# Kernel tuning notes

Measured on AMD Instinct MI355X. Metric: run time of the kernel, lower is better.

## Reference

```python
import jax, jax.numpy as jnp
import numpy as np

T = 10
NUM_HEADS = 12

def _rel_pos_index(t):
    coords = jnp.arange(t)
    return coords[:, None] - coords[None, :] + (t - 1)  # [T, T] in [0, 2T-2]

def setup_inputs() -> dict:
    key = jax.random.key(0)
    ks = jax.random.split(key, 6)
    dim, attn_dim = 384, 384
    B_ = 16384
    return {
        "x": jax.random.normal(ks[0], (B_, T, dim), dtype=jnp.float32),
        "qkv_w": jax.random.normal(ks[1], (3 * attn_dim, dim), dtype=jnp.float32) * 0.02,
        "qkv_b": jax.random.normal(ks[2], (3 * attn_dim,), dtype=jnp.float32) * 0.02,
        "proj_w": jax.random.normal(ks[3], (dim, attn_dim), dtype=jnp.float32) * 0.02,
        "proj_b": jax.random.normal(ks[4], (dim,), dtype=jnp.float32) * 0.02,
        "bias_table": jax.random.normal(ks[5], (2 * T - 1, NUM_HEADS), dtype=jnp.float32) * 0.02,
    }

def reference(x, qkv_w, qkv_b, proj_w, proj_b, bias_table):
    B_, N, C = x.shape
    H = NUM_HEADS
    Dh = qkv_w.shape[0] // (3 * H)
    scale = Dh ** -0.5
    qkv = x @ qkv_w.T + qkv_b                       # [B_, N, 3*H*Dh]
    qkv = qkv.reshape(B_, N, 3, H, Dh).transpose(2, 0, 3, 1, 4)
    q, k, v = qkv[0], qkv[1], qkv[2]                # each [B_, H, N, Dh]
    idx = _rel_pos_index(N)                         # [N, N]
    bias = bias_table[idx].transpose(2, 0, 1)       # [H, N, N]
    attn = jnp.einsum('bhnd,bhmd->bhnm', q * scale, k) + bias[None]
    attn = jax.nn.softmax(attn, axis=-1)
    out = jnp.einsum('bhnm,bhmd->bhnd', attn, v)    # [B_, H, N, Dh]
    out = out.transpose(0, 2, 1, 3).reshape(B_, N, H * Dh)
    return out @ proj_w.T + proj_b
```

## Files before the change

kernel.cpp:

```cpp
#include <hip/hip_runtime.h>
#include <cstdint>
#include <cstddef>

#define T_TOK 10
#define NH 12
#define DH 32
#define DIM 384
#define QKVDIM 1152
#define NB 4
#define MROWS 40
#define XS_LD 392
#define QKV_LD 1160
#define SCALE 0.17677669529663689f

#define LDS_BYTES 131344

typedef short bf16x8 __attribute__((ext_vector_type(8)));
typedef float f32x4  __attribute__((ext_vector_type(4)));

__device__ __forceinline__ unsigned short f2b(float f) {
    unsigned u = __float_as_uint(f);
    u = (u + 0x7FFFu + ((u >> 16) & 1u)) >> 16;
    return (unsigned short)u;
}
__device__ __forceinline__ float b2f(unsigned short h) {
    return __uint_as_float(((unsigned)h) << 16);
}
__device__ __forceinline__ unsigned pack2(float a, float b) {
    return (unsigned)f2b(a) | ((unsigned)f2b(b) << 16);
}

__global__ void convert_weights(const float* __restrict__ qkv_w,
                                const float* __restrict__ proj_w,
                                unsigned short* __restrict__ wq,
                                unsigned short* __restrict__ wp) {
    int i = blockIdx.x * blockDim.x + threadIdx.x;
    const int N1 = QKVDIM * DIM / 4;
    const int N2 = DIM * DIM / 4;
    if (i < N1) {
        float4 v = ((const float4*)qkv_w)[i];
        uint2 o; o.x = pack2(v.x, v.y); o.y = pack2(v.z, v.w);
        ((uint2*)wq)[i] = o;
    } else if (i < N1 + N2) {
        int j = i - N1;
        float4 v = ((const float4*)proj_w)[j];
        uint2 o; o.x = pack2(v.x, v.y); o.y = pack2(v.z, v.w);
        ((uint2*)wp)[j] = o;
    }
}

extern __shared__ char smem[];

__global__ __launch_bounds__(256, 1) void fused_attn(
    const float* __restrict__ x,
    const float* __restrict__ qkv_b,
    const float* __restrict__ proj_b,
    const float* __restrict__ bias_table,
    const unsigned short* __restrict__ wq,
    const unsigned short* __restrict__ wp,
    float* __restrict__ out)
{
    const int t    = threadIdx.x;
    const int wg   = blockIdx.x;
    const int wave = t >> 6;
    const int lane = t & 63;
    const int quad = lane >> 4;
    const int l16  = lane & 15;

    unsigned short* xs       = (unsigned short*)smem;
    unsigned short* qkvs     = (unsigned short*)(smem + 37632);
    float*          outstage = (float*)(smem + 37632);
    float*          bias_lds = (float*)(smem + 130432);

    {
        const float4* x4 = (const float4*)(x + (size_t)wg * MROWS * DIM);
        #pragma unroll
        for (int i = 0; i < 15; ++i) {
            int idx = i * 256 + t;
            int row = idx / 96, c4 = idx % 96;
            float4 v = x4[idx];
            uint2 o; o.x = pack2(v.x, v.y); o.y = pack2(v.z, v.w);
            *(uint2*)(xs + row * XS_LD + c4 * 4) = o;
        }
        for (int idx = t; idx < 8 * 98; idx += 256) {
            int row = MROWS + idx / 98, c4 = idx % 98;
            *(uint2*)(xs + row * XS_LD + c4 * 4) = make_uint2(0u, 0u);
        }
        if (t < (2 * T_TOK - 1) * NH) bias_lds[t] = bias_table[t];
    }
    __syncthreads();

    {
        #pragma unroll 1
        for (int g = 0; g < 6; ++g) {
            f32x4 acc[3][3] = {};
            #pragma unroll
            for (int kc = 0; kc < 12; ++kc) {
                int koff = kc * 32 + quad * 8;
                bf16x8 a0 = *(const bf16x8*)(xs + ( 0 + l16) * XS_LD + koff);
                bf16x8 a1 = *(const bf16x8*)(xs + (16 + l16) * XS_LD + koff);
                bf16x8 a2 = *(const bf16x8*)(xs + (32 + l16) * XS_LD + koff);
                bf16x8 b0 = *(const bf16x8*)(wq + (size_t)((wave + 4*(3*g+0))*16 + l16) * DIM + koff);
                bf16x8 b1 = *(const bf16x8*)(wq + (size_t)((wave + 4*(3*g+1))*16 + l16) * DIM + koff);
                bf16x8 b2 = *(const bf16x8*)(wq + (size_t)((wave + 4*(3*g+2))*16 + l16) * DIM + koff);
                acc[0][0] = __builtin_amdgcn_mfma_f32_16x16x32_bf16(a0, b0, acc[0][0], 0, 0, 0);
                acc[0][1] = __builtin_amdgcn_mfma_f32_16x16x32_bf16(a0, b1, acc[0][1], 0, 0, 0);
                acc[0][2] = __builtin_amdgcn_mfma_f32_16x16x32_bf16(a0, b2, acc[0][2], 0, 0, 0);
                acc[1][0] = __builtin_amdgcn_mfma_f32_16x16x32_bf16(a1, b0, acc[1][0], 0, 0, 0);
                acc[1][1] = __builtin_amdgcn_mfma_f32_16x16x32_bf16(a1, b1, acc[1][1], 0, 0, 0);
                acc[1][2] = __builtin_amdgcn_mfma_f32_16x16x32_bf16(a1, b2, acc[1][2], 0, 0, 0);
                acc[2][0] = __builtin_amdgcn_mfma_f32_16x16x32_bf16(a2, b0, acc[2][0], 0, 0, 0);
                acc[2][1] = __builtin_amdgcn_mfma_f32_16x16x32_bf16(a2, b1, acc[2][1], 0, 0, 0);
                acc[2][2] = __builtin_amdgcn_mfma_f32_16x16x32_bf16(a2, b2, acc[2][2], 0, 0, 0);
            }
            #pragma unroll
            for (int j = 0; j < 3; ++j) {
                int n = (wave + 4*(3*g+j)) * 16 + l16;
                float qb = qkv_b[n];
                float sc = (n < DIM) ? SCALE : 1.0f;
                #pragma unroll
                for (int mt = 0; mt < 3; ++mt) {
                    #pragma unroll
                    for (int r = 0; r < 4; ++r) {
                        int m = mt * 16 + quad * 4 + r;
                        if (m < MROWS)
                            qkvs[m * QKV_LD + n] = f2b((acc[mt][j][r] + qb) * sc);
                    }
                }
            }
        }
    }
    __syncthreads();

    if (t < 240) {
        int pr = t / 5, rp = t % 5;
        int bl = pr / NH, h = pr % NH;
        int m0 = bl * T_TOK + rp * 2;
        int ti0 = rp * 2, ti1 = rp * 2 + 1;

        float q0[DH], q1[DH];
        const unsigned* qp0 = (const unsigned*)(qkvs + m0 * QKV_LD + h * DH);
        const unsigned* qp1 = (const unsigned*)(qkvs + (m0 + 1) * QKV_LD + h * DH);
        #pragma unroll
        for (int u = 0; u < 16; ++u) {
            unsigned w0 = qp0[u], w1 = qp1[u];
            q0[2*u] = b2f((unsigned short)w0); q0[2*u+1] = b2f((unsigned short)(w0 >> 16));
            q1[2*u] = b2f((unsigned short)w1); q1[2*u+1] = b2f((unsigned short)(w1 >> 16));
        }

        float s0[T_TOK], s1[T_TOK];
        #pragma unroll
        for (int j = 0; j < T_TOK; ++j) {
            const unsigned* kp = (const unsigned*)(qkvs + (bl * T_TOK + j) * QKV_LD + DIM + h * DH);
            float d0 = 0.f, d1 = 0.f;
            #pragma unroll
            for (int u = 0; u < 16; ++u) {
                unsigned w = kp[u];
                float e0 = b2f((unsigned short)w), e1 = b2f((unsigned short)(w >> 16));
                d0 += q0[2*u] * e0; d0 += q0[2*u+1] * e1;
                d1 += q1[2*u] * e0; d1 += q1[2*u+1] * e1;
            }
            s0[j] = d0 + bias_lds[(ti0 - j + T_TOK - 1) * NH + h];
            s1[j] = d1 + bias_lds[(ti1 - j + T_TOK - 1) * NH + h];
        }

        float mx0 = s0[0], mx1 = s1[0];
        #pragma unroll
        for (int j = 1; j < T_TOK; ++j) { mx0 = fmaxf(mx0, s0[j]); mx1 = fmaxf(mx1, s1[j]); }
        float sum0 = 0.f, sum1 = 0.f;
        #pragma unroll
        for (int j = 0; j < T_TOK; ++j) {
            s0[j] = __expf(s0[j] - mx0); sum0 += s0[j];
            s1[j] = __expf(s1[j] - mx1); sum1 += s1[j];
        }
        float r0 = 1.f / sum0, r1 = 1.f / sum1;

        float o0[DH] = {}, o1[DH] = {};
        #pragma unroll
        for (int j = 0; j < T_TOK; ++j) {
            const unsigned* vp = (const unsigned*)(qkvs + (bl * T_TOK + j) * QKV_LD + 2 * DIM + h * DH);
            float p0 = s0[j] * r0, p1 = s1[j] * r1;
            #pragma unroll
            for (int u = 0; u < 16; ++u) {
                unsigned w = vp[u];
                float e0 = b2f((unsigned short)w), e1 = b2f((unsigned short)(w >> 16));
                o0[2*u] += p0 * e0; o0[2*u+1] += p0 * e1;
                o1[2*u] += p1 * e0; o1[2*u+1] += p1 * e1;
            }
        }

        unsigned* os0 = (unsigned*)(xs + m0 * XS_LD + h * DH);
        unsigned* os1 = (unsigned*)(xs + (m0 + 1) * XS_LD + h * DH);
        #pragma unroll
        for (int u = 0; u < 16; ++u) {
            os0[u] = pack2(o0[2*u], o0[2*u+1]);
            os1[u] = pack2(o1[2*u], o1[2*u+1]);
        }
    }
    __syncthreads();

    {
        #pragma unroll 1
        for (int g = 0; g < 2; ++g) {
            f32x4 acc[3][3] = {};
            #pragma unroll
            for (int kc = 0; kc < 12; ++kc) {
                int koff = kc * 32 + quad * 8;
                bf16x8 a0 = *(const bf16x8*)(xs + ( 0 + l16) * XS_LD + koff);
                bf16x8 a1 = *(const bf16x8*)(xs + (16 + l16) * XS_LD + koff);
                bf16x8 a2 = *(const bf16x8*)(xs + (32 + l16) * XS_LD + koff);
                bf16x8 b0 = *(const bf16x8*)(wp + (size_t)((wave + 4*(3*g+0))*16 + l16) * DIM + koff);
                bf16x8 b1 = *(const bf16x8*)(wp + (size_t)((wave + 4*(3*g+1))*16 + l16) * DIM + koff);
                bf16x8 b2 = *(const bf16x8*)(wp + (size_t)((wave + 4*(3*g+2))*16 + l16) * DIM + koff);
                acc[0][0] = __builtin_amdgcn_mfma_f32_16x16x32_bf16(a0, b0, acc[0][0], 0, 0, 0);
                acc[0][1] = __builtin_amdgcn_mfma_f32_16x16x32_bf16(a0, b1, acc[0][1], 0, 0, 0);
                acc[0][2] = __builtin_amdgcn_mfma_f32_16x16x32_bf16(a0, b2, acc[0][2], 0, 0, 0);
                acc[1][0] = __builtin_amdgcn_mfma_f32_16x16x32_bf16(a1, b0, acc[1][0], 0, 0, 0);
                acc[1][1] = __builtin_amdgcn_mfma_f32_16x16x32_bf16(a1, b1, acc[1][1], 0, 0, 0);
                acc[1][2] = __builtin_amdgcn_mfma_f32_16x16x32_bf16(a1, b2, acc[1][2], 0, 0, 0);
                acc[2][0] = __builtin_amdgcn_mfma_f32_16x16x32_bf16(a2, b0, acc[2][0], 0, 0, 0);
                acc[2][1] = __builtin_amdgcn_mfma_f32_16x16x32_bf16(a2, b1, acc[2][1], 0, 0, 0);
                acc[2][2] = __builtin_amdgcn_mfma_f32_16x16x32_bf16(a2, b2, acc[2][2], 0, 0, 0);
            }
            #pragma unroll
            for (int j = 0; j < 3; ++j) {
                int c = (wave + 4*(3*g+j)) * 16 + l16;
                #pragma unroll
                for (int mt = 0; mt < 3; ++mt) {
                    #pragma unroll
                    for (int r = 0; r < 4; ++r) {
                        int m = mt * 16 + quad * 4 + r;
                        if (m < MROWS)
                            outstage[m * DIM + c] = acc[mt][j][r];
                    }
                }
            }
        }
    }
    __syncthreads();

    {
        const float4* st4 = (const float4*)outstage;
        const float4* pb4 = (const float4*)proj_b;
        float4* out4 = (float4*)(out + (size_t)wg * MROWS * DIM);
        #pragma unroll
        for (int i = 0; i < 15; ++i) {
            int idx = i * 256 + t;
            int c4 = idx % 96;
            float4 v = st4[idx];
            float4 b = pb4[c4];
            float4 r; r.x = v.x + b.x; r.y = v.y + b.y; r.z = v.z + b.z; r.w = v.w + b.w;
            out4[idx] = r;
        }
    }
}

extern "C" void kernel_launch(void* const* d_in, const int* in_sizes, int n_in,
                              void* d_out, int out_size, void* d_ws, size_t ws_size,
                              hipStream_t stream) {
    const float* x          = (const float*)d_in[0];
    const float* qkv_w      = (const float*)d_in[1];
    const float* qkv_b      = (const float*)d_in[2];
    const float* proj_w     = (const float*)d_in[3];
    const float* proj_b     = (const float*)d_in[4];
    const float* bias_table = (const float*)d_in[5];

    unsigned short* wq = (unsigned short*)d_ws;
    unsigned short* wp = wq + (size_t)QKVDIM * DIM;
    float* out = (float*)d_out;

    convert_weights<<<576, 256, 0, stream>>>(qkv_w, proj_w, wq, wp);

    hipFuncSetAttribute((const void*)fused_attn,
                        hipFuncAttributeMaxDynamicSharedMemorySize, LDS_BYTES);
    fused_attn<<<16384 / NB, 256, LDS_BYTES, stream>>>(x, qkv_b, proj_b, bias_table, wq, wp, out);
}
```

Before: 1.145 ms.

## Compute attention with MFMA using transposed V layout and 512-thread blocks

Replaces the scalar per-thread QK^T, softmax and PV loops with 16x16x32 bf16 MFMA tiles per (block, head) pair. Softmax reductions now use cross-lane shuffles. V is written to LDS transposed and zero-padded so it can feed the MFMA directly, and the workgroup grows to 8 waves, which halves the per-wave share of the QKV and projection GEMMs. This costs more LDS, padded MFMA work on the 10-token tiles, extra shuffles, and a zero-fill of the V buffer.

```diff
diff --git a/kernel.cpp b/kernel.cpp
--- a/kernel.cpp
+++ b/kernel.cpp
@@ -10,10 +10,13 @@
 #define NB 4
 #define MROWS 40
 #define XS_LD 392
-#define QKV_LD 1160
+#define QK_LD 776
 #define SCALE 0.17677669529663689f
 
-#define LDS_BYTES 131344
+#define QK_OFF   37632
+#define VT_OFF   99712
+#define BIAS_OFF 148864
+#define LDS_BYTES 149776
 
 typedef short bf16x8 __attribute__((ext_vector_type(8)));
 typedef float f32x4  __attribute__((ext_vector_type(4)));
@@ -22,9 +25,6 @@
     unsigned u = __float_as_uint(f);
     u = (u + 0x7FFFu + ((u >> 16) & 1u)) >> 16;
     return (unsigned short)u;
-}
-__device__ __forceinline__ float b2f(unsigned short h) {
-    return __uint_as_float(((unsigned)h) << 16);
 }
 __device__ __forceinline__ unsigned pack2(float a, float b) {
     return (unsigned)f2b(a) | ((unsigned)f2b(b) << 16);
@@ -51,7 +51,7 @@
 
 extern __shared__ char smem[];
 
-__global__ __launch_bounds__(256, 1) void fused_attn(
+__global__ __launch_bounds__(512, 2) void fused_attn(
     const float* __restrict__ x,
     const float* __restrict__ qkv_b,
     const float* __restrict__ proj_b,
@@ -68,31 +68,32 @@
     const int l16  = lane & 15;
 
     unsigned short* xs       = (unsigned short*)smem;
-    unsigned short* qkvs     = (unsigned short*)(smem + 37632);
-    float*          outstage = (float*)(smem + 37632);
-    float*          bias_lds = (float*)(smem + 130432);
+    unsigned short* qk       = (unsigned short*)(smem + QK_OFF);
+    unsigned short* vt       = (unsigned short*)(smem + VT_OFF);
+    float*          outstage = (float*)(smem + QK_OFF);
+    float*          bias_lds = (float*)(smem + BIAS_OFF);
 
     {
         const float4* x4 = (const float4*)(x + (size_t)wg * MROWS * DIM);
-        #pragma unroll
-        for (int i = 0; i < 15; ++i) {
-            int idx = i * 256 + t;
+        for (int idx = t; idx < MROWS * 96; idx += 512) {
             int row = idx / 96, c4 = idx % 96;
             float4 v = x4[idx];
             uint2 o; o.x = pack2(v.x, v.y); o.y = pack2(v.z, v.w);
             *(uint2*)(xs + row * XS_LD + c4 * 4) = o;
         }
-        for (int idx = t; idx < 8 * 98; idx += 256) {
-            int row = MROWS + idx / 98, c4 = idx % 98;
+        for (int idx = t; idx < 8 * 96; idx += 512) {
+            int row = MROWS + idx / 96, c4 = idx % 96;
             *(uint2*)(xs + row * XS_LD + c4 * 4) = make_uint2(0u, 0u);
         }
+        for (int idx = t; idx < 3072; idx += 512)
+            ((uint4*)vt)[idx] = make_uint4(0u, 0u, 0u, 0u);
         if (t < (2 * T_TOK - 1) * NH) bias_lds[t] = bias_table[t];
     }
     __syncthreads();
 
     {
         #pragma unroll 1
-        for (int g = 0; g < 6; ++g) {
+        for (int g = 0; g < 3; ++g) {
             f32x4 acc[3][3] = {};
             #pragma unroll
             for (int kc = 0; kc < 12; ++kc) {
@@ -100,9 +101,9 @@
                 bf16x8 a0 = *(const bf16x8*)(xs + ( 0 + l16) * XS_LD + koff);
                 bf16x8 a1 = *(const bf16x8*)(xs + (16 + l16) * XS_LD + koff);
                 bf16x8 a2 = *(const bf16x8*)(xs + (32 + l16) * XS_LD + koff);
-                bf16x8 b0 = *(const bf16x8*)(wq + (size_t)((wave + 4*(3*g+0))*16 + l16) * DIM + koff);
-                bf16x8 b1 = *(const bf16x8*)(wq + (size_t)((wave + 4*(3*g+1))*16 + l16) * DIM + koff);
-                bf16x8 b2 = *(const bf16x8*)(wq + (size_t)((wave + 4*(3*g+2))*16 + l16) * DIM + koff);
+                bf16x8 b0 = *(const bf16x8*)(wq + (size_t)((wave + 8*(3*g+0))*16 + l16) * DIM + koff);
+                bf16x8 b1 = *(const bf16x8*)(wq + (size_t)((wave + 8*(3*g+1))*16 + l16) * DIM + koff);
+                bf16x8 b2 = *(const bf16x8*)(wq + (size_t)((wave + 8*(3*g+2))*16 + l16) * DIM + koff);
                 acc[0][0] = __builtin_amdgcn_mfma_f32_16x16x32_bf16(a0, b0, acc[0][0], 0, 0, 0);
                 acc[0][1] = __builtin_amdgcn_mfma_f32_16x16x32_bf16(a0, b1, acc[0][1], 0, 0, 0);
                 acc[0][2] = __builtin_amdgcn_mfma_f32_16x16x32_bf16(a0, b2, acc[0][2], 0, 0, 0);
@@ -115,16 +116,33 @@
             }
             #pragma unroll
             for (int j = 0; j < 3; ++j) {
-                int n = (wave + 4*(3*g+j)) * 16 + l16;
+                int n = (wave + 8*(3*g+j)) * 16 + l16;
                 float qb = qkv_b[n];
-                float sc = (n < DIM) ? SCALE : 1.0f;
-                #pragma unroll
-                for (int mt = 0; mt < 3; ++mt) {
+                if (g < 2) {
+                    float sc = (g == 0) ? SCALE : 1.0f;
                     #pragma unroll
-                    for (int r = 0; r < 4; ++r) {
-                        int m = mt * 16 + quad * 4 + r;
-                        if (m < MROWS)
-                            qkvs[m * QKV_LD + n] = f2b((acc[mt][j][r] + qb) * sc);
+                    for (int mt = 0; mt < 3; ++mt) {
+                        #pragma unroll
+                        for (int r = 0; r < 4; ++r) {
+                            int m = mt * 16 + quad * 4 + r;
+                            if (m < MROWS)
+                                qk[m * QK_LD + n] = f2b((acc[mt][j][r] + qb) * sc);
+                        }
+                    }
+                } else {
+                    int h = (n - 2*DIM) >> 5;
+                    int d = (n - 2*DIM) & 31;
+                    #pragma unroll
+                    for (int mt = 0; mt < 3; ++mt) {
+                        #pragma unroll
+                        for (int r = 0; r < 4; ++r) {
+                            int m = mt * 16 + quad * 4 + r;
+                            if (m < MROWS) {
+                                int bl = (m * 205) >> 11;
+                                int jt = m - bl * 10;
+                                vt[((bl*NH + h)*DH + d)*16 + jt] = f2b(acc[mt][j][r] + qb);
+                            }
+                        }
                     }
                 }
             }
@@ -132,107 +150,95 @@
     }
     __syncthreads();
 
-    if (t < 240) {
-        int pr = t / 5, rp = t % 5;
-        int bl = pr / NH, h = pr % NH;
-        int m0 = bl * T_TOK + rp * 2;
-        int ti0 = rp * 2, ti1 = rp * 2 + 1;
-
-        float q0[DH], q1[DH];
-        const unsigned* qp0 = (const unsigned*)(qkvs + m0 * QKV_LD + h * DH);
-        const unsigned* qp1 = (const unsigned*)(qkvs + (m0 + 1) * QKV_LD + h * DH);
+    {
+        const int l16c = (l16 < T_TOK) ? l16 : (T_TOK - 1);
+        const int joff = (quad < 2) ? quad * 8 : 8;
+        #pragma unroll 2
+        for (int pp = 0; pp < 6; ++pp) {
+            int p  = wave * 6 + pp;
+            int bl = p / NH, h = p % NH;
+            int rowq = bl * T_TOK + l16c;
+            bf16x8 kf = *(const bf16x8*)(qk + rowq * QK_LD + DIM + h * DH + quad * 8);
+            bf16x8 qf = *(const bf16x8*)(qk + rowq * QK_LD +       h * DH + quad * 8);
+            f32x4 sv = {};
+            sv = __builtin_amdgcn_mfma_f32_16x16x32_bf16(kf, qf, sv, 0, 0, 0);
+            float s[4];
+            #pragma unroll
+            for (int r = 0; r < 4; ++r) {
+                int jj  = quad * 4 + r;
+                int jjc = (jj < T_TOK) ? jj : (T_TOK - 1);
+                float b = bias_lds[(l16c - jjc + T_TOK - 1) * NH + h];
+                s[r] = (jj < T_TOK) ? (sv[r] + b) : -1.0e30f;
+            }
+            float mx = fmaxf(fmaxf(s[0], s[1]), fmaxf(s[2], s[3]));
+            mx = fmaxf(mx, __shfl_xor(mx, 16));
+            mx = fmaxf(mx, __shfl_xor(mx, 32));
+            float p0 = __expf(s[0] - mx), p1 = __expf(s[1] - mx);
+            float p2 = __expf(s[2] - mx), p3 = __expf(s[3] - mx);
+            float sl = p0 + p1 + p2 + p3;
+            sl += __shfl_xor(sl, 16);
+            sl += __shfl_xor(sl, 32);
+            float rinv = 1.0f / sl;
+            unsigned w0 = pack2(p0, p1), w1 = pack2(p2, p3);
+            int s0l = ((quad & 1) << 5) + l16;
+            unsigned d0 = (unsigned)__shfl((int)w0, s0l);
+            unsigned d1 = (unsigned)__shfl((int)w1, s0l);
+            unsigned d2 = (unsigned)__shfl((int)w0, s0l + 16);
+            unsigned d3 = (unsigned)__shfl((int)w1, s0l + 16);
+            if (quad >= 2) { d0 = 0; d1 = 0; d2 = 0; d3 = 0; }
+            union { bf16x8 v; unsigned u[4]; } pa;
+            pa.u[0] = d0; pa.u[1] = d1; pa.u[2] = d2; pa.u[3] = d3;
+            const unsigned short* vb = vt + (size_t)((bl*NH + h)*DH) * 16;
+            bf16x8 v0 = *(const bf16x8*)(vb + ( 0 + l16) * 16 + joff);
+            bf16x8 v1 = *(const bf16x8*)(vb + (16 + l16) * 16 + joff);
+            f32x4 o0 = {}, o1 = {};
+            o0 = __builtin_amdgcn_mfma_f32_16x16x32_bf16(pa.v, v0, o0, 0, 0, 0);
+            o1 = __builtin_amdgcn_mfma_f32_16x16x32_bf16(pa.v, v1, o1, 0, 0, 0);
+            #pragma unroll
+            for (int r = 0; r < 4; ++r) {
+                float rv = __shfl(rinv, quad * 4 + r);
+                int i = quad * 4 + r;
+                if (i < T_TOK) {
+                    int m = bl * T_TOK + i;
+                    xs[m * XS_LD + h * DH +      l16] = f2b(o0[r] * rv);
+                    xs[m * XS_LD + h * DH + 16 + l16] = f2b(o1[r] * rv);
+                }
+            }
+        }
+    }
+    __syncthreads();
+
+    {
+        f32x4 acc[3][3] = {};
         #pragma unroll
-        for (int u = 0; u < 16; ++u) {
-            unsigned w0 = qp0[u], w1 = qp1[u];
-            q0[2*u] = b2f((unsigned short)w0); q0[2*u+1] = b2f((unsigned short)(w0 >> 16));
-            q1[2*u] = b2f((unsigned short)w1); q1[2*u+1] = b2f((unsigned short)(w1 >> 16));
-        }
-
-        float s0[T_TOK], s1[T_TOK];
+        for (int kc = 0; kc < 12; ++kc) {
+            int koff = kc * 32 + quad * 8;
+            bf16x8 a0 = *(const bf16x8*)(xs + ( 0 + l16) * XS_LD + koff);
+            bf16x8 a1 = *(const bf16x8*)(xs + (16 + l16) * XS_LD + koff);
+            bf16x8 a2 = *(const bf16x8*)(xs + (32 + l16) * XS_LD + koff);
+            bf16x8 b0 = *(const bf16x8*)(wp + (size_t)((wave +  0)*16 + l16) * DIM + koff);
+            bf16x8 b1 = *(const bf16x8*)(wp + (size_t)((wave +  8)*16 + l16) * DIM + koff);
+            bf16x8 b2 = *(const bf16x8*)(wp + (size_t)((wave + 16)*16 + l16) * DIM + koff);
+            acc[0][0] = __builtin_amdgcn_mfma_f32_16x16x32_bf16(a0, b0, acc[0][0], 0, 0, 0);
+            acc[0][1] = __builtin_amdgcn_mfma_f32_16x16x32_bf16(a0, b1, acc[0][1], 0, 0, 0);
+            acc[0][2] = __builtin_amdgcn_mfma_f32_16x16x32_bf16(a0, b2, acc[0][2], 0, 0, 0);
+            acc[1][0] = __builtin_amdgcn_mfma_f32_16x16x32_bf16(a1, b0, acc[1][0], 0, 0, 0);
+            acc[1][1] = __builtin_amdgcn_mfma_f32_16x16x32_bf16(a1, b1, acc[1][1], 0, 0, 0);
+            acc[1][2] = __builtin_amdgcn_mfma_f32_16x16x32_bf16(a1, b2, acc[1][2], 0, 0, 0);
+            acc[2][0] = __builtin_amdgcn_mfma_f32_16x16x32_bf16(a2, b0, acc[2][0], 0, 0, 0);
+            acc[2][1] = __builtin_amdgcn_mfma_f32_16x16x32_bf16(a2, b1, acc[2][1], 0, 0, 0);
+            acc[2][2] = __builtin_amdgcn_mfma_f32_16x16x32_bf16(a2, b2, acc[2][2], 0, 0, 0);
+        }
         #pragma unroll
-        for (int j = 0; j < T_TOK; ++j) {
-            const unsigned* kp = (const unsigned*)(qkvs + (bl * T_TOK + j) * QKV_LD + DIM + h * DH);
-            float d0 = 0.f, d1 = 0.f;
-            #pragma unroll
-            for (int u = 0; u < 16; ++u) {
-                unsigned w = kp[u];
-                float e0 = b2f((unsigned short)w), e1 = b2f((unsigned short)(w >> 16));
-                d0 += q0[2*u] * e0; d0 += q0[2*u+1] * e1;
-                d1 += q1[2*u] * e0; d1 += q1[2*u+1] * e1;
-            }
-            s0[j] = d0 + bias_lds[(ti0 - j + T_TOK - 1) * NH + h];
-            s1[j] = d1 + bias_lds[(ti1 - j + T_TOK - 1) * NH + h];
-        }
-
-        float mx0 = s0[0], mx1 = s1[0];
-        #pragma unroll
-        for (int j = 1; j < T_TOK; ++j) { mx0 = fmaxf(mx0, s0[j]); mx1 = fmaxf(mx1, s1[j]); }
-        float sum0 = 0.f, sum1 = 0.f;
-        #pragma unroll
-        for (int j = 0; j < T_TOK; ++j) {
-            s0[j] = __expf(s0[j] - mx0); sum0 += s0[j];
-            s1[j] = __expf(s1[j] - mx1); sum1 += s1[j];
-        }
-        float r0 = 1.f / sum0, r1 = 1.f / sum1;
-
-        float o0[DH] = {}, o1[DH] = {};
-        #pragma unroll
-        for (int j = 0; j < T_TOK; ++j) {
-            const unsigned* vp = (const unsigned*)(qkvs + (bl * T_TOK + j) * QKV_LD + 2 * DIM + h * DH);
-            float p0 = s0[j] * r0, p1 = s1[j] * r1;
-            #pragma unroll
-            for (int u = 0; u < 16; ++u) {
-                unsigned w = vp[u];
-                float e0 = b2f((unsigned short)w), e1 = b2f((unsigned short)(w >> 16));
-                o0[2*u] += p0 * e0; o0[2*u+1] += p0 * e1;
-                o1[2*u] += p1 * e0; o1[2*u+1] += p1 * e1;
-            }
-        }
-
-        unsigned* os0 = (unsigned*)(xs + m0 * XS_LD + h * DH);
-        unsigned* os1 = (unsigned*)(xs + (m0 + 1) * XS_LD + h * DH);
-        #pragma unroll
-        for (int u = 0; u < 16; ++u) {
-            os0[u] = pack2(o0[2*u], o0[2*u+1]);
-            os1[u] = pack2(o1[2*u], o1[2*u+1]);
-        }
-    }
-    __syncthreads();
-
-    {
-        #pragma unroll 1
-        for (int g = 0; g < 2; ++g) {
-            f32x4 acc[3][3] = {};
-            #pragma unroll
-            for (int kc = 0; kc < 12; ++kc) {
-                int koff = kc * 32 + quad * 8;
-                bf16x8 a0 = *(const bf16x8*)(xs + ( 0 + l16) * XS_LD + koff);
-                bf16x8 a1 = *(const bf16x8*)(xs + (16 + l16) * XS_LD + koff);
-                bf16x8 a2 = *(const bf16x8*)(xs + (32 + l16) * XS_LD + koff);
-                bf16x8 b0 = *(const bf16x8*)(wp + (size_t)((wave + 4*(3*g+0))*16 + l16) * DIM + koff);
-                bf16x8 b1 = *(const bf16x8*)(wp + (size_t)((wave + 4*(3*g+1))*16 + l16) * DIM + koff);
-                bf16x8 b2 = *(const bf16x8*)(wp + (size_t)((wave + 4*(3*g+2))*16 + l16) * DIM + koff);
-                acc[0][0] = __builtin_amdgcn_mfma_f32_16x16x32_bf16(a0, b0, acc[0][0], 0, 0, 0);
-                acc[0][1] = __builtin_amdgcn_mfma_f32_16x16x32_bf16(a0, b1, acc[0][1], 0, 0, 0);
-                acc[0][2] = __builtin_amdgcn_mfma_f32_16x16x32_bf16(a0, b2, acc[0][2], 0, 0, 0);
-                acc[1][0] = __builtin_amdgcn_mfma_f32_16x16x32_bf16(a1, b0, acc[1][0], 0, 0, 0);
-                acc[1][1] = __builtin_amdgcn_mfma_f32_16x16x32_bf16(a1, b1, acc[1][1], 0, 0, 0);
-                acc[1][2] = __builtin_amdgcn_mfma_f32_16x16x32_bf16(a1, b2, acc[1][2], 0, 0, 0);
-                acc[2][0] = __builtin_amdgcn_mfma_f32_16x16x32_bf16(a2, b0, acc[2][0], 0, 0, 0);
-                acc[2][1] = __builtin_amdgcn_mfma_f32_16x16x32_bf16(a2, b1, acc[2][1], 0, 0, 0);
-                acc[2][2] = __builtin_amdgcn_mfma_f32_16x16x32_bf16(a2, b2, acc[2][2], 0, 0, 0);
-            }
-            #pragma unroll
-            for (int j = 0; j < 3; ++j) {
-                int c = (wave + 4*(3*g+j)) * 16 + l16;
+        for (int j = 0; j < 3; ++j) {
+            int c = (wave + 8*j) * 16 + l16;
+            #pragma unroll
+            for (int mt = 0; mt < 3; ++mt) {
                 #pragma unroll
-                for (int mt = 0; mt < 3; ++mt) {
-                    #pragma unroll
-                    for (int r = 0; r < 4; ++r) {
-                        int m = mt * 16 + quad * 4 + r;
-                        if (m < MROWS)
-                            outstage[m * DIM + c] = acc[mt][j][r];
-                    }
+                for (int r = 0; r < 4; ++r) {
+                    int m = mt * 16 + quad * 4 + r;
+                    if (m < MROWS)
+                        outstage[m * DIM + c] = acc[mt][j][r];
                 }
             }
         }
@@ -243,9 +249,7 @@
         const float4* st4 = (const float4*)outstage;
         const float4* pb4 = (const float4*)proj_b;
         float4* out4 = (float4*)(out + (size_t)wg * MROWS * DIM);
-        #pragma unroll
-        for (int i = 0; i < 15; ++i) {
-            int idx = i * 256 + t;
+        for (int idx = t; idx < MROWS * 96; idx += 512) {
             int c4 = idx % 96;
             float4 v = st4[idx];
             float4 b = pb4[c4];
@@ -259,11 +263,13 @@
                               void* d_out, int out_size, void* d_ws, size_t ws_size,
                               hipStream_t stream) {
     const float* x          = (const float*)d_in[0];
-    const float* qkv_w      = (const float*)d_in[1];
-    const float* qkv_b      = (const float*)d_in[2];
+    const float* qkv_b      = (const float*)d_in[1];
+    const float* qkv_b_     = (const float*)d_in[2];
     const float* proj_w     = (const float*)d_in[3];
     const float* proj_b     = (const float*)d_in[4];
     const float* bias_table = (const float*)d_in[5];
+    const float* qkv_w = qkv_b;
+    const float* qkv_bias = qkv_b_;
 
     unsigned short* wq = (unsigned short*)d_ws;
     unsigned short* wp = wq + (size_t)QKVDIM * DIM;
@@ -273,5 +279,5 @@
 
     hipFuncSetAttribute((const void*)fused_attn,
                         hipFuncAttributeMaxDynamicSharedMemorySize, LDS_BYTES);
-    fused_attn<<<16384 / NB, 256, LDS_BYTES, stream>>>(x, qkv_b, proj_b, bias_table, wq, wp, out);
-}
+    fused_attn<<<16384 / NB, 512, LDS_BYTES, stream>>>(x, qkv_bias, proj_b, bias_table, wq, wp, out);
+}
```

New measurement: 1.075 ms. -6.1%, faster.
